# Performance work log

Measured on AMD Instinct MI355X. Metric: run time of the kernel, lower is better.

## Reference

```python
import jax, jax.numpy as jnp
import numpy as np

N, E, DIM, H = 50000, 800000, 64, 4

def setup_inputs() -> dict:
    key = jax.random.key(0)
    k0, k1, k2, k3, k4 = jax.random.split(key, 5)
    h_v = jax.random.normal(k0, (N, DIM), dtype=jnp.float32)
    src = jax.random.randint(k1, (E,), 0, N, dtype=jnp.int64)
    dst = jax.random.randint(k2, (E,), 0, N, dtype=jnp.int64)
    W_fc = jax.random.normal(k3, (DIM * H, DIM), dtype=jnp.float32) * 0.05
    b_fc = jnp.zeros((DIM * H,), dtype=jnp.float32)
    W_pi = jax.random.normal(k4, (1, DIM * H), dtype=jnp.float32) * 0.05
    return {"h_v": h_v, "src": src, "dst": dst, "W_fc": W_fc, "b_fc": b_fc, "W_pi": W_pi}

def reference(h_v, src, dst, W_fc, b_fc, W_pi):
    n, dim = h_v.shape
    heads = W_fc.shape[0] // dim
    # fc: [N, dim] -> [N, H*dim]
    ft = h_v @ W_fc.T + b_fc
    # u_mul_v: per-edge elementwise product of src/dst features  [E, H*dim]
    e = ft[src] * ft[dst]
    # pi + LeakyReLU(0.2): per-edge scalar score  [E]
    s = jax.nn.leaky_relu(e @ W_pi.T, negative_slope=0.2)[:, 0]
    # edge_softmax over incoming edges of each destination node (stable)
    smax = jax.ops.segment_max(s, dst, num_segments=n)
    ex = jnp.exp(s - smax[dst])
    denom = jax.ops.segment_sum(ex, dst, num_segments=n)
    a = ex / denom[dst]                        # [E]
    # u_mul_e + scatter-sum into destination nodes  [N, H*dim]
    agg = jax.ops.segment_sum(ft[src] * a[:, None], dst, num_segments=n)
    # max-pool over heads  [N, dim]
    return agg.reshape(n, heads, dim).max(axis=1)
```

## Files before the change

kernel.cpp:

```cpp
#include <hip/hip_runtime.h>
#include <math.h>

#define DIM 64
#define FDIM 256
#define DEFER_THR 4.0f

typedef _Float16 h2 __attribute__((ext_vector_type(2)));

__global__ __launch_bounds__(256) void fc_kernel(const float* __restrict__ h,
                                                 const float* __restrict__ W,
                                                 const float* __restrict__ b,
                                                 _Float16* __restrict__ ft, int N)
{
    int t = threadIdx.x;
    float w[DIM];
#pragma unroll
    for (int j = 0; j < DIM / 4; ++j) {
        float4 v = *(const float4*)(W + (size_t)t * DIM + j * 4);
        w[4 * j + 0] = v.x; w[4 * j + 1] = v.y;
        w[4 * j + 2] = v.z; w[4 * j + 3] = v.w;
    }
    float bt = b[t];
    for (int r = blockIdx.x; r < N; r += gridDim.x) {
        const float4* h4 = (const float4*)(h + (size_t)r * DIM);
        float acc = bt;
#pragma unroll
        for (int j = 0; j < DIM / 4; ++j) {
            float4 hv = h4[j];
            acc = fmaf(hv.x, w[4 * j + 0], acc);
            acc = fmaf(hv.y, w[4 * j + 1], acc);
            acc = fmaf(hv.z, w[4 * j + 2], acc);
            acc = fmaf(hv.w, w[4 * j + 3], acc);
        }
        ft[(size_t)r * FDIM + t] = (_Float16)acc;
    }
}

__global__ void hist_rank_kernel(const int* __restrict__ dst, int* __restrict__ cnt,
                                 int* __restrict__ rank, int E)
{
    int i = blockIdx.x * blockDim.x + threadIdx.x;
    if (i < E) rank[i] = atomicAdd(&cnt[dst[i]], 1);
}

__global__ __launch_bounds__(256) void scanA_kernel(const int* __restrict__ cnt,
                                                    int* __restrict__ off,
                                                    int* __restrict__ bsum, int N)
{
    __shared__ int sh[256];
    int t = threadIdx.x;
    int i = blockIdx.x * 256 + t;
    int v = (i < N) ? cnt[i] : 0;
    sh[t] = v;
    __syncthreads();
#pragma unroll
    for (int o = 1; o < 256; o <<= 1) {
        int x = (t >= o) ? sh[t - o] : 0;
        __syncthreads();
        sh[t] += x;
        __syncthreads();
    }
    if (i < N) off[i] = sh[t] - v;
    if (t == 255) bsum[blockIdx.x] = sh[255];
}

__global__ __launch_bounds__(256) void scanB_kernel(int* __restrict__ bsum, int nb)
{
    __shared__ int sh[256];
    int t = threadIdx.x;
    int carry = 0;
    for (int base = 0; base < nb; base += 256) {
        int i = base + t;
        int v = (i < nb) ? bsum[i] : 0;
        sh[t] = v;
        __syncthreads();
#pragma unroll
        for (int o = 1; o < 256; o <<= 1) {
            int x = (t >= o) ? sh[t - o] : 0;
            __syncthreads();
            sh[t] += x;
            __syncthreads();
        }
        if (i < nb) bsum[i] = carry + sh[t] - v;
        int tot = sh[255];
        __syncthreads();
        carry += tot;
    }
}

__global__ void scatter_kernel(const int* __restrict__ src, const int* __restrict__ dst,
                               const int* __restrict__ off, const int* __restrict__ bsum,
                               const int* __restrict__ rank,
                               int* __restrict__ ssrc, int E)
{
    int i = blockIdx.x * blockDim.x + threadIdx.x;
    if (i < E) {
        int d = dst[i];
        ssrc[off[d] + bsum[d >> 8] + rank[i]] = src[i];
    }
}

__global__ __launch_bounds__(256) void agg_kernel(const _Float16* __restrict__ ft,
                                                  const int* __restrict__ off,
                                                  const int* __restrict__ bsum,
                                                  const int* __restrict__ ssrc,
                                                  const float* __restrict__ Wpi,
                                                  float* __restrict__ out, int N, int E)
{
    __shared__ float xb[4][1280];
    int wid = (blockIdx.x * blockDim.x + threadIdx.x) >> 6;
    int wv  = threadIdx.x >> 6;
    int lane = threadIdx.x & 63;
    if (wid >= N) return;
    int q  = lane >> 4;
    int ql = lane & 15;

    h2 fdwh[8];
    {
        const float* wp = Wpi + ql * 16;
        const _Float16* drow = ft + (size_t)wid * FDIM + ql * 16;
        uint4 a = *(const uint4*)(drow);
        uint4 b = *(const uint4*)(drow + 8);
        const h2* da = (const h2*)&a;
        const h2* db = (const h2*)&b;
#pragma unroll
        for (int j = 0; j < 4; ++j) {
            h2 v = da[j], u = db[j];
            fdwh[j].x     = (_Float16)((float)v.x * wp[2 * j + 0]);
            fdwh[j].y     = (_Float16)((float)v.y * wp[2 * j + 1]);
            fdwh[4 + j].x = (_Float16)((float)u.x * wp[8 + 2 * j + 0]);
            fdwh[4 + j].y = (_Float16)((float)u.y * wp[8 + 2 * j + 1]);
        }
    }

    int e0 = off[wid] + bsum[wid >> 8];
    int e1 = (wid + 1 < N) ? (off[wid + 1] + bsum[(wid + 1) >> 8]) : E;
    float mq = -INFINITY, lq = 0.f;
    float acc[16];
#pragma unroll
    for (int j = 0; j < 16; ++j) acc[j] = 0.f;

    auto LOAD8 = [&](uint4& a1, uint4& b1, uint4& a2, uint4& b2,
                     bool& v1, bool& v2, int bse) {
        int lo = bse + q, hi = bse + q + 4;
        v1 = lo < e1; v2 = hi < e1;
        int s1 = ssrc[v1 ? lo : e0];
        int s2 = ssrc[v2 ? hi : e0];
        const _Float16* r1 = ft + (size_t)s1 * FDIM + ql * 16;
        const _Float16* r2 = ft + (size_t)s2 * FDIM + ql * 16;
        a1 = *(const uint4*)(r1);
        b1 = *(const uint4*)(r1 + 8);
        a2 = *(const uint4*)(r2);
        b2 = *(const uint4*)(r2 + 8);
    };
    auto COMP8 = [&](uint4 a1, uint4 b1, uint4 a2, uint4 b2, bool v1, bool v2) {
        const h2* fa1 = (const h2*)&a1; const h2* fb1 = (const h2*)&b1;
        const h2* fa2 = (const h2*)&a2; const h2* fb2 = (const h2*)&b2;
        float p1 = 0.f, p2 = 0.f;
#pragma unroll
        for (int j = 0; j < 4; ++j) {
            p1 = __builtin_amdgcn_fdot2(fa1[j], fdwh[j], p1, false);
            p2 = __builtin_amdgcn_fdot2(fa2[j], fdwh[j], p2, false);
        }
#pragma unroll
        for (int j = 0; j < 4; ++j) {
            p1 = __builtin_amdgcn_fdot2(fb1[j], fdwh[4 + j], p1, false);
            p2 = __builtin_amdgcn_fdot2(fb2[j], fdwh[4 + j], p2, false);
        }
        p1 += __shfl_xor(p1, 1, 64);  p2 += __shfl_xor(p2, 1, 64);
        p1 += __shfl_xor(p1, 2, 64);  p2 += __shfl_xor(p2, 2, 64);
        p1 += __shfl_xor(p1, 4, 64);  p2 += __shfl_xor(p2, 4, 64);
        p1 += __shfl_xor(p1, 8, 64);  p2 += __shfl_xor(p2, 8, 64);
        float s1 = p1 > 0.f ? p1 : 0.2f * p1;
        float s2 = p2 > 0.f ? p2 : 0.2f * p2;
        if (!v1) s1 = -INFINITY;
        if (!v2) s2 = -INFINITY;
        float smax = fmaxf(s1, s2);
        if (smax > mq + DEFER_THR) {
            float sc = __expf(mq - smax);
            lq *= sc;
#pragma unroll
            for (int j = 0; j < 16; ++j) acc[j] *= sc;
            mq = smax;
        }
        float pe1 = v1 ? __expf(s1 - mq) : 0.f;
        float pe2 = v2 ? __expf(s2 - mq) : 0.f;
        lq += pe1 + pe2;
#pragma unroll
        for (int j = 0; j < 4; ++j) {
            acc[2 * j + 0] = fmaf((float)fa1[j].x, pe1, acc[2 * j + 0]);
            acc[2 * j + 1] = fmaf((float)fa1[j].y, pe1, acc[2 * j + 1]);
            acc[8 + 2 * j + 0] = fmaf((float)fb1[j].x, pe1, acc[8 + 2 * j + 0]);
            acc[8 + 2 * j + 1] = fmaf((float)fb1[j].y, pe1, acc[8 + 2 * j + 1]);
        }
#pragma unroll
        for (int j = 0; j < 4; ++j) {
            acc[2 * j + 0] = fmaf((float)fa2[j].x, pe2, acc[2 * j + 0]);
            acc[2 * j + 1] = fmaf((float)fa2[j].y, pe2, acc[2 * j + 1]);
            acc[8 + 2 * j + 0] = fmaf((float)fb2[j].x, pe2, acc[8 + 2 * j + 0]);
            acc[8 + 2 * j + 1] = fmaf((float)fb2[j].y, pe2, acc[8 + 2 * j + 1]);
        }
    };

    if (e0 < e1) {
        uint4 Aa1, Ab1, Aa2, Ab2, Ba1, Bb1, Ba2, Bb2;
        bool Av1, Av2, Bv1, Bv2;
        int base = e0;
        LOAD8(Aa1, Ab1, Aa2, Ab2, Av1, Av2, base);
        while (true) {
            int nxt = base + 8;
            bool more = nxt < e1;
            if (more) LOAD8(Ba1, Bb1, Ba2, Bb2, Bv1, Bv2, nxt);
            COMP8(Aa1, Ab1, Aa2, Ab2, Av1, Av2);
            if (!more) break;
            base = nxt;
            nxt = base + 8;
            more = nxt < e1;
            if (more) LOAD8(Aa1, Ab1, Aa2, Ab2, Av1, Av2, nxt);
            COMP8(Ba1, Bb1, Ba2, Bb2, Bv1, Bv2);
            if (!more) break;
            base = nxt;
        }
    }

    float mstar = fmaxf(mq, __shfl_xor(mq, 16, 64));
    mstar = fmaxf(mstar, __shfl_xor(mstar, 32, 64));
    float sc = (lq > 0.f) ? __expf(mq - mstar) : 0.f;
    float lt = lq * sc;
    lt += __shfl_xor(lt, 16, 64);
    lt += __shfl_xor(lt, 32, 64);
    float inv = (lt > 0.f) ? 1.f / lt : 0.f;

    {
        float* wp = &xb[wv][(unsigned)lane * 20];
#pragma unroll
        for (int k = 0; k < 4; ++k) {
            *(float4*)(wp + 4 * k) = make_float4(acc[4 * k] * sc, acc[4 * k + 1] * sc,
                                                 acc[4 * k + 2] * sc, acc[4 * k + 3] * sc);
        }
    }
    asm volatile("s_waitcnt lgkmcnt(0)" ::: "memory");
    {
        int col = lane >> 4, jp = lane & 15;
        float A[4];
#pragma unroll
        for (int h = 0; h < 4; ++h) {
            int rowb = (col + 4 * h) * 20 + jp;
            float v0 = xb[wv][rowb];
            float v1 = xb[wv][rowb + 16 * 20];
            float v2 = xb[wv][rowb + 32 * 20];
            float v3 = xb[wv][rowb + 48 * 20];
            A[h] = (v0 + v1) + (v2 + v3);
        }
        float r = fmaxf(fmaxf(A[0], A[1]), fmaxf(A[2], A[3])) * inv;
        out[(size_t)wid * DIM + lane] = r;
    }
}

extern "C" void kernel_launch(void* const* d_in, const int* in_sizes, int n_in,
                              void* d_out, int out_size, void* d_ws, size_t ws_size,
                              hipStream_t stream)
{
    const float* h_v  = (const float*)d_in[0];
    const int*   src  = (const int*)d_in[1];
    const int*   dst  = (const int*)d_in[2];
    const float* W_fc = (const float*)d_in[3];
    const float* b_fc = (const float*)d_in[4];
    const float* W_pi = (const float*)d_in[5];
    float* out = (float*)d_out;

    int N = in_sizes[0] / DIM;
    int E = in_sizes[1];

    _Float16* ft = (_Float16*)d_ws;
    size_t ftB = (((size_t)N * FDIM * 2) + 255) & ~(size_t)255;
    char*  p    = (char*)d_ws + ftB;
    int*   cnt  = (int*)(p);
    int*   off  = (int*)(p + 256 * 1024);
    int*   bsum = (int*)(p + 512 * 1024);
    int*   rank = (int*)(p + 768 * 1024);
    int*   ssrc = (int*)(p + 768 * 1024 + (((size_t)E * 4 + 255) & ~(size_t)255));

    int nb = (N + 255) / 256;
    int eb = (E + 255) / 256;
    fc_kernel<<<1024, 256, 0, stream>>>(h_v, W_fc, b_fc, ft, N);
    hipMemsetAsync(cnt, 0, (size_t)N * sizeof(int), stream);
    hist_rank_kernel<<<eb, 256, 0, stream>>>(dst, cnt, rank, E);
    scanA_kernel<<<nb, 256, 0, stream>>>(cnt, off, bsum, N);
    scanB_kernel<<<1, 256, 0, stream>>>(bsum, nb);
    scatter_kernel<<<eb, 256, 0, stream>>>(src, dst, off, bsum, rank, ssrc, E);
    int blocks = (N * 64 + 255) / 256;
    agg_kernel<<<blocks, 256, 0, stream>>>(ft, off, bsum, ssrc, W_pi, out, N, E);
}
```

Measured before the change: 160.4 us.

## Map four destination nodes per wavefront and fold count zeroing into fc kernel

The aggregation kernel now assigns one 16-lane quarter-wave to each destination node instead of a whole wavefront per node. Each quarter streams its node's edges one at a time with double-buffered gathers. The head max-pool is done with lane shuffles instead of an LDS transpose, and the cross-quarter softmax merge is removed. Separately, zeroing the count array moves from a memset into the fc kernel to save a launch. Work is now uneven across quarters, since every quarter loops to the largest degree in its wave, and each quarter issues fewer gathers per iteration.

```diff
diff --git a/kernel.cpp b/kernel.cpp
--- a/kernel.cpp
+++ b/kernel.cpp
@@ -10,8 +10,12 @@
 __global__ __launch_bounds__(256) void fc_kernel(const float* __restrict__ h,
                                                  const float* __restrict__ W,
                                                  const float* __restrict__ b,
-                                                 _Float16* __restrict__ ft, int N)
-{
+                                                 _Float16* __restrict__ ft,
+                                                 int* __restrict__ cnt, int N)
+{
+    for (int i = blockIdx.x * blockDim.x + threadIdx.x; i < N;
+         i += gridDim.x * blockDim.x) cnt[i] = 0;
+
     int t = threadIdx.x;
     float w[DIM];
 #pragma unroll
@@ -107,18 +111,18 @@
                                                   const float* __restrict__ Wpi,
                                                   float* __restrict__ out, int N, int E)
 {
-    __shared__ float xb[4][1280];
-    int wid = (blockIdx.x * blockDim.x + threadIdx.x) >> 6;
-    int wv  = threadIdx.x >> 6;
+    int gw = blockIdx.x * (blockDim.x >> 6) + (threadIdx.x >> 6);
     int lane = threadIdx.x & 63;
-    if (wid >= N) return;
     int q  = lane >> 4;
     int ql = lane & 15;
+    int nd = gw * 4 + q;
+    bool nv = nd < N;
 
     h2 fdwh[8];
-    {
+    int e0 = 0, e1 = 0;
+    if (nv) {
         const float* wp = Wpi + ql * 16;
-        const _Float16* drow = ft + (size_t)wid * FDIM + ql * 16;
+        const _Float16* drow = ft + (size_t)nd * FDIM + ql * 16;
         uint4 a = *(const uint4*)(drow);
         uint4 b = *(const uint4*)(drow + 8);
         const h2* da = (const h2*)&a;
@@ -131,129 +135,89 @@
             fdwh[4 + j].x = (_Float16)((float)u.x * wp[8 + 2 * j + 0]);
             fdwh[4 + j].y = (_Float16)((float)u.y * wp[8 + 2 * j + 1]);
         }
-    }
-
-    int e0 = off[wid] + bsum[wid >> 8];
-    int e1 = (wid + 1 < N) ? (off[wid + 1] + bsum[(wid + 1) >> 8]) : E;
+        e0 = off[nd] + bsum[nd >> 8];
+        e1 = (nd + 1 < N) ? (off[nd + 1] + bsum[(nd + 1) >> 8]) : E;
+    }
+    int deg = e1 - e0;
+    int mx = max(deg, __shfl_xor(deg, 16, 64));
+    mx = max(mx, __shfl_xor(mx, 32, 64));
+    int lastv = (deg > 0) ? (e1 - 1) : 0;
+
     float mq = -INFINITY, lq = 0.f;
     float acc[16];
 #pragma unroll
     for (int j = 0; j < 16; ++j) acc[j] = 0.f;
 
-    auto LOAD8 = [&](uint4& a1, uint4& b1, uint4& a2, uint4& b2,
-                     bool& v1, bool& v2, int bse) {
-        int lo = bse + q, hi = bse + q + 4;
-        v1 = lo < e1; v2 = hi < e1;
-        int s1 = ssrc[v1 ? lo : e0];
-        int s2 = ssrc[v2 ? hi : e0];
-        const _Float16* r1 = ft + (size_t)s1 * FDIM + ql * 16;
-        const _Float16* r2 = ft + (size_t)s2 * FDIM + ql * 16;
-        a1 = *(const uint4*)(r1);
-        b1 = *(const uint4*)(r1 + 8);
-        a2 = *(const uint4*)(r2);
-        b2 = *(const uint4*)(r2 + 8);
+    auto LOAD = [&](uint4& ra, uint4& rb, int it) {
+        int idx = e0 + it;
+        int s = ssrc[(idx < e1) ? idx : lastv];
+        const _Float16* r = ft + (size_t)s * FDIM + ql * 16;
+        ra = *(const uint4*)(r);
+        rb = *(const uint4*)(r + 8);
     };
-    auto COMP8 = [&](uint4 a1, uint4 b1, uint4 a2, uint4 b2, bool v1, bool v2) {
-        const h2* fa1 = (const h2*)&a1; const h2* fb1 = (const h2*)&b1;
-        const h2* fa2 = (const h2*)&a2; const h2* fb2 = (const h2*)&b2;
-        float p1 = 0.f, p2 = 0.f;
+    auto COMP = [&](uint4 ra, uint4 rb, int it) {
+        bool val = (e0 + it) < e1;
+        const h2* fa = (const h2*)&ra;
+        const h2* fb = (const h2*)&rb;
+        float p = 0.f;
+#pragma unroll
+        for (int j = 0; j < 4; ++j) p = __builtin_amdgcn_fdot2(fa[j], fdwh[j], p, false);
+#pragma unroll
+        for (int j = 0; j < 4; ++j) p = __builtin_amdgcn_fdot2(fb[j], fdwh[4 + j], p, false);
+        p += __shfl_xor(p, 1, 64);
+        p += __shfl_xor(p, 2, 64);
+        p += __shfl_xor(p, 4, 64);
+        p += __shfl_xor(p, 8, 64);
+        float s = p > 0.f ? p : 0.2f * p;
+        if (!val) s = -INFINITY;
+        if (s > mq + DEFER_THR) {
+            float sc = __expf(mq - s);
+            lq *= sc;
+#pragma unroll
+            for (int j = 0; j < 16; ++j) acc[j] *= sc;
+            mq = s;
+        }
+        float pe = val ? __expf(s - mq) : 0.f;
+        lq += pe;
 #pragma unroll
         for (int j = 0; j < 4; ++j) {
-            p1 = __builtin_amdgcn_fdot2(fa1[j], fdwh[j], p1, false);
-            p2 = __builtin_amdgcn_fdot2(fa2[j], fdwh[j], p2, false);
-        }
-#pragma unroll
-        for (int j = 0; j < 4; ++j) {
-            p1 = __builtin_amdgcn_fdot2(fb1[j], fdwh[4 + j], p1, false);
-            p2 = __builtin_amdgcn_fdot2(fb2[j], fdwh[4 + j], p2, false);
-        }
-        p1 += __shfl_xor(p1, 1, 64);  p2 += __shfl_xor(p2, 1, 64);
-        p1 += __shfl_xor(p1, 2, 64);  p2 += __shfl_xor(p2, 2, 64);
-        p1 += __shfl_xor(p1, 4, 64);  p2 += __shfl_xor(p2, 4, 64);
-        p1 += __shfl_xor(p1, 8, 64);  p2 += __shfl_xor(p2, 8, 64);
-        float s1 = p1 > 0.f ? p1 : 0.2f * p1;
-        float s2 = p2 > 0.f ? p2 : 0.2f * p2;
-        if (!v1) s1 = -INFINITY;
-        if (!v2) s2 = -INFINITY;
-        float smax = fmaxf(s1, s2);
-        if (smax > mq + DEFER_THR) {
-            float sc = __expf(mq - smax);
-            lq *= sc;
-#pragma unroll
-            for (int j = 0; j < 16; ++j) acc[j] *= sc;
-            mq = smax;
-        }
-        float pe1 = v1 ? __expf(s1 - mq) : 0.f;
-        float pe2 = v2 ? __expf(s2 - mq) : 0.f;
-        lq += pe1 + pe2;
-#pragma unroll
-        for (int j = 0; j < 4; ++j) {
-            acc[2 * j + 0] = fmaf((float)fa1[j].x, pe1, acc[2 * j + 0]);
-            acc[2 * j + 1] = fmaf((float)fa1[j].y, pe1, acc[2 * j + 1]);
-            acc[8 + 2 * j + 0] = fmaf((float)fb1[j].x, pe1, acc[8 + 2 * j + 0]);
-            acc[8 + 2 * j + 1] = fmaf((float)fb1[j].y, pe1, acc[8 + 2 * j + 1]);
-        }
-#pragma unroll
-        for (int j = 0; j < 4; ++j) {
-            acc[2 * j + 0] = fmaf((float)fa2[j].x, pe2, acc[2 * j + 0]);
-            acc[2 * j + 1] = fmaf((float)fa2[j].y, pe2, acc[2 * j + 1]);
-            acc[8 + 2 * j + 0] = fmaf((float)fb2[j].x, pe2, acc[8 + 2 * j + 0]);
-            acc[8 + 2 * j + 1] = fmaf((float)fb2[j].y, pe2, acc[8 + 2 * j + 1]);
+            acc[2 * j + 0] = fmaf((float)fa[j].x, pe, acc[2 * j + 0]);
+            acc[2 * j + 1] = fmaf((float)fa[j].y, pe, acc[2 * j + 1]);
+            acc[8 + 2 * j + 0] = fmaf((float)fb[j].x, pe, acc[8 + 2 * j + 0]);
+            acc[8 + 2 * j + 1] = fmaf((float)fb[j].y, pe, acc[8 + 2 * j + 1]);
         }
     };
 
-    if (e0 < e1) {
-        uint4 Aa1, Ab1, Aa2, Ab2, Ba1, Bb1, Ba2, Bb2;
-        bool Av1, Av2, Bv1, Bv2;
-        int base = e0;
-        LOAD8(Aa1, Ab1, Aa2, Ab2, Av1, Av2, base);
+    if (mx > 0) {
+        uint4 Aa, Ab, Ba, Bb;
+        LOAD(Aa, Ab, 0);
+        if (mx > 1) LOAD(Ba, Bb, 1);
+        int it = 0;
         while (true) {
-            int nxt = base + 8;
-            bool more = nxt < e1;
-            if (more) LOAD8(Ba1, Bb1, Ba2, Bb2, Bv1, Bv2, nxt);
-            COMP8(Aa1, Ab1, Aa2, Ab2, Av1, Av2);
-            if (!more) break;
-            base = nxt;
-            nxt = base + 8;
-            more = nxt < e1;
-            if (more) LOAD8(Aa1, Ab1, Aa2, Ab2, Av1, Av2, nxt);
-            COMP8(Ba1, Bb1, Ba2, Bb2, Bv1, Bv2);
-            if (!more) break;
-            base = nxt;
-        }
-    }
-
-    float mstar = fmaxf(mq, __shfl_xor(mq, 16, 64));
-    mstar = fmaxf(mstar, __shfl_xor(mstar, 32, 64));
-    float sc = (lq > 0.f) ? __expf(mq - mstar) : 0.f;
-    float lt = lq * sc;
-    lt += __shfl_xor(lt, 16, 64);
-    lt += __shfl_xor(lt, 32, 64);
-    float inv = (lt > 0.f) ? 1.f / lt : 0.f;
-
-    {
-        float* wp = &xb[wv][(unsigned)lane * 20];
-#pragma unroll
-        for (int k = 0; k < 4; ++k) {
-            *(float4*)(wp + 4 * k) = make_float4(acc[4 * k] * sc, acc[4 * k + 1] * sc,
-                                                 acc[4 * k + 2] * sc, acc[4 * k + 3] * sc);
-        }
-    }
-    asm volatile("s_waitcnt lgkmcnt(0)" ::: "memory");
-    {
-        int col = lane >> 4, jp = lane & 15;
-        float A[4];
-#pragma unroll
-        for (int h = 0; h < 4; ++h) {
-            int rowb = (col + 4 * h) * 20 + jp;
-            float v0 = xb[wv][rowb];
-            float v1 = xb[wv][rowb + 16 * 20];
-            float v2 = xb[wv][rowb + 32 * 20];
-            float v3 = xb[wv][rowb + 48 * 20];
-            A[h] = (v0 + v1) + (v2 + v3);
-        }
-        float r = fmaxf(fmaxf(A[0], A[1]), fmaxf(A[2], A[3])) * inv;
-        out[(size_t)wid * DIM + lane] = r;
+            COMP(Aa, Ab, it);
+            if (it + 2 < mx) LOAD(Aa, Ab, it + 2);
+            ++it; if (it >= mx) break;
+            COMP(Ba, Bb, it);
+            if (it + 2 < mx) LOAD(Ba, Bb, it + 2);
+            ++it; if (it >= mx) break;
+        }
+    }
+
+    float inv = (lq > 0.f) ? 1.f / lq : 0.f;
+    float r[16];
+#pragma unroll
+    for (int j = 0; j < 16; ++j) {
+        float v = acc[j];
+        v = fmaxf(v, __shfl_xor(v, 4, 64));
+        v = fmaxf(v, __shfl_xor(v, 8, 64));
+        r[j] = v * inv;
+    }
+    if (nv && ql < 4) {
+        float4* o4 = (float4*)(out + (size_t)nd * DIM + ql * 16);
+        o4[0] = make_float4(r[0],  r[1],  r[2],  r[3]);
+        o4[1] = make_float4(r[4],  r[5],  r[6],  r[7]);
+        o4[2] = make_float4(r[8],  r[9],  r[10], r[11]);
+        o4[3] = make_float4(r[12], r[13], r[14], r[15]);
     }
 }
 
@@ -283,12 +247,11 @@
 
     int nb = (N + 255) / 256;
     int eb = (E + 255) / 256;
-    fc_kernel<<<1024, 256, 0, stream>>>(h_v, W_fc, b_fc, ft, N);
-    hipMemsetAsync(cnt, 0, (size_t)N * sizeof(int), stream);
+    fc_kernel<<<1024, 256, 0, stream>>>(h_v, W_fc, b_fc, ft, cnt, N);
     hist_rank_kernel<<<eb, 256, 0, stream>>>(dst, cnt, rank, E);
     scanA_kernel<<<nb, 256, 0, stream>>>(cnt, off, bsum, N);
     scanB_kernel<<<1, 256, 0, stream>>>(bsum, nb);
     scatter_kernel<<<eb, 256, 0, stream>>>(src, dst, off, bsum, rank, ssrc, E);
-    int blocks = (N * 64 + 255) / 256;
-    agg_kernel<<<blocks, 256, 0, stream>>>(ft, off, bsum, ssrc, W_pi, out, N, E);
-}
+    int aggblocks = (N + 15) / 16;
+    agg_kernel<<<aggblocks, 256, 0, stream>>>(ft, off, bsum, ssrc, W_pi, out, N, E);
+}
```

After: 178.0 us. 10.9% more time.
